# Kernel tuning notes

Hardware: AMD Instinct MI355X
Metric: run time of the kernel (lower is better)

The kernel has to match this reference:

```python
import jax, jax.numpy as jnp
import numpy as np

B = 4096
SEQ = 128            # window_size * rnn_in_pkts
WINDOW = 32
IN_PKTS = 4
LEN_V, LEN_E = 1500, 64
IPD_V, IPD_E = 256, 64
EV = 64              # embedding_vector_bits
RNN_IN = IN_PKTS * EV   # 256
H = 256              # rnn_hidden_bits
LABELS = 100


def setup_inputs() -> dict:
    key = jax.random.key(0)
    ks = jax.random.split(key, 12)
    s = 0.05
    return {
        "len_x": jax.random.randint(ks[0], (B, SEQ), 0, LEN_V),
        "ipd_x": jax.random.randint(ks[1], (B, SEQ), 0, IPD_V),
        "len_emb": jax.random.normal(ks[2], (LEN_V, LEN_E), jnp.float32) * s,
        "ipd_emb": jax.random.normal(ks[3], (IPD_V, IPD_E), jnp.float32) * s,
        "fc_w": jax.random.normal(ks[4], (EV, LEN_E + IPD_E), jnp.float32) * s,
        "fc_b": jax.random.normal(ks[5], (EV,), jnp.float32) * s,
        "w_ih": jax.random.normal(ks[6], (3 * H, RNN_IN), jnp.float32) * s,
        "w_hh": jax.random.normal(ks[7], (3 * H, H), jnp.float32) * s,
        "b_ih": jax.random.normal(ks[8], (3 * H,), jnp.float32) * s,
        "b_hh": jax.random.normal(ks[9], (3 * H,), jnp.float32) * s,
        "out_w": jax.random.normal(ks[10], (LABELS, H), jnp.float32) * s,
        "out_b": jax.random.normal(ks[11], (LABELS,), jnp.float32) * s,
    }


def _gru_scan(rnn_in, w_ih, w_hh, b_ih, b_hh):
    # rnn_in: [B, T, RNN_IN]. Precompute input-side gates for all steps at once.
    gi_all = jnp.einsum("bti,gi->btg", rnn_in, w_ih) + b_ih  # [B,T,3H]
    h0 = jnp.zeros((rnn_in.shape[0], H), rnn_in.dtype)

    def step(h, gi):
        gh = h @ w_hh.T + b_hh                 # [B,3H]
        i_r, i_z, i_n = jnp.split(gi, 3, axis=-1)
        h_r, h_z, h_n = jnp.split(gh, 3, axis=-1)
        r = jax.nn.sigmoid(i_r + h_r)
        z = jax.nn.sigmoid(i_z + h_z)
        n = jnp.tanh(i_n + r * h_n)
        h_new = (1.0 - z) * n + z * h
        return h_new, None

    h_final, _ = jax.lax.scan(step, h0, jnp.swapaxes(gi_all, 0, 1))
    return h_final


def reference(len_x, ipd_x, len_emb, ipd_emb, fc_w, fc_b, w_ih, w_hh, b_ih, b_hh, out_w, out_b):
    len_e = len_emb[len_x]                      # [B,SEQ,LEN_E]
    ipd_e = ipd_emb[ipd_x]                      # [B,SEQ,IPD_E]
    cat = jnp.concatenate([len_e, ipd_e], axis=-1)
    evs = cat @ fc_w.T + fc_b                   # [B,SEQ,EV]
    rnn_in = evs.reshape(B, WINDOW, RNN_IN)     # [B,32,256]
    h = _gru_scan(rnn_in, w_ih, w_hh, b_ih, b_hh)
    logits = h @ out_w.T + out_b                # [B,LABELS]
    return logits
```

## Files before the change

kernel.cpp:

```cpp
#include <hip/hip_runtime.h>
#include <hip/hip_bf16.h>

typedef __bf16 bf16_t;
typedef __bf16 bf16x8 __attribute__((ext_vector_type(8)));
typedef float f32x4 __attribute__((ext_vector_type(4)));
typedef unsigned short u16x4 __attribute__((ext_vector_type(4)));

#define MFMA16(a, b, c) __builtin_amdgcn_mfma_f32_16x16x32_bf16((a), (b), (c), 0, 0, 0)

#define BATCH 4096
#define SEQN 128
#define HN 256
#define NLABELS 100
#define TSTEPS 32
#define LEN_VN 1500
#define IPD_VN 256

#define OFF_LENT   0u
#define OFF_IPDT   384000u
#define OFF_WIH    449536u
#define OFF_WHH    842752u
#define OFF_GI     1235968u

__device__ __forceinline__ float sigf(float x) {
    return __builtin_amdgcn_rcpf(1.f + __expf(-x));
}
__device__ __forceinline__ float tanh_fast(float x) {
    return 2.f * __builtin_amdgcn_rcpf(1.f + __expf(-2.f * x)) - 1.f;
}
__device__ __forceinline__ float b2f(unsigned short v) {
    union { unsigned u; float f; } c; c.u = ((unsigned)v) << 16; return c.f;
}
__device__ __forceinline__ f32x4 b2f4(u16x4 v) {
    f32x4 o;
    #pragma unroll
    for (int r = 0; r < 4; ++r) o[r] = b2f(v[r]);
    return o;
}
__device__ __forceinline__ unsigned short f2b(float f) {
    union { bf16_t h; unsigned short s; } c; c.h = (bf16_t)f; return c.s;
}

__device__ __forceinline__ void barrier_lds() {
    asm volatile("s_waitcnt lgkmcnt(0)\n\ts_barrier" ::: "memory");
}
__device__ __forceinline__ void wait_vm0() {
    asm volatile("s_waitcnt vmcnt(0)" ::: "memory");
}

#define PREP_TBL_BLOCKS 110
__global__ void prep_kernel(const float* __restrict__ len_emb,
                            const float* __restrict__ ipd_emb,
                            const float* __restrict__ fc_w,
                            const float* __restrict__ fc_b,
                            const float* __restrict__ w_ih,
                            const float* __restrict__ w_hh,
                            float* __restrict__ lenT, float* __restrict__ ipdT,
                            bf16_t* __restrict__ wfrag_ih,
                            bf16_t* __restrict__ wfrag_hh) {
    const int bid = blockIdx.x, tid = threadIdx.x;
    if (bid < PREP_TBL_BLOCKS) {
        __shared__ float w_lds[64 * 132];
        __shared__ float emb_lds[16 * 64];
        const int row0 = bid * 16;

        #pragma unroll
        for (int k = 0; k < 8; ++k) {
            const int l = k * 1024 + tid * 4;
            const int e = l >> 7, j = l & 127;
            *(f32x4*)(w_lds + e * 132 + j) = *(const f32x4*)(fc_w + l);
        }
        {
            const int r = tid >> 4;
            const int c = (tid & 15) * 4;
            const int grow = row0 + r;
            f32x4 v = {};
            if (grow < LEN_VN)               v = *(const f32x4*)(len_emb + grow * 64 + c);
            else if (grow < LEN_VN + IPD_VN) v = *(const f32x4*)(ipd_emb + (grow - LEN_VN) * 64 + c);
            *(f32x4*)(emb_lds + r * 64 + c) = v;
        }
        __syncthreads();

        const int e = tid & 63;
        const int r0 = tid >> 6;
        const float* wrow_lo = w_lds + e * 132;
        #pragma unroll
        for (int rr = 0; rr < 4; ++rr) {
            const int r = r0 + rr * 4;
            const int grow = row0 + r;
            if (grow >= LEN_VN + IPD_VN) break;
            const bool is_len = grow < LEN_VN;
            const float* wrow = is_len ? wrow_lo : (wrow_lo + 64);
            f32x4 acc = {};
            #pragma unroll
            for (int c = 0; c < 16; ++c) {
                f32x4 wv = *(const f32x4*)(wrow + c * 4);
                f32x4 ev = *(const f32x4*)(emb_lds + r * 64 + c * 4);
                acc += wv * ev;
            }
            float s = acc[0] + acc[1] + acc[2] + acc[3] + (is_len ? fc_b[e] : 0.f);
            if (is_len) lenT[grow * 64 + e] = s;
            else        ipdT[(grow - LEN_VN) * 64 + e] = s;
        }
    } else {
        const int flat = (bid - PREP_TBL_BLOCKS) * 256 + tid;
        const int which = flat / 24576;
        const int rem = flat % 24576;
        const int c = rem >> 9;
        const int kt = (rem >> 6) & 7;
        const int lane = rem & 63;
        const int g = c * 16 + (lane & 15);
        const int k0 = kt * 32 + (lane >> 4) * 8;
        const float* src = (which == 0 ? w_ih : w_hh) + g * 256 + k0;
        bf16_t* dst = (which == 0 ? wfrag_ih : wfrag_hh) + ((c * 8 + kt) * 64 + lane) * 8;
        f32x4 s0 = *(const f32x4*)(src);
        f32x4 s1 = *(const f32x4*)(src + 4);
        bf16x8 o;
        #pragma unroll
        for (int j = 0; j < 4; ++j) { o[j] = (bf16_t)s0[j]; o[4 + j] = (bf16_t)s1[j]; }
        *(bf16x8*)dst = o;
    }
}

__global__ void __launch_bounds__(1024, 4)
fused_kernel(const int* __restrict__ len_x, const int* __restrict__ ipd_x,
             const float* __restrict__ lenT, const float* __restrict__ ipdT,
             const bf16_t* __restrict__ wfrag_ih,
             const bf16_t* __restrict__ wfrag_hh,
             const float* __restrict__ b_ih, const float* __restrict__ b_hh,
             bf16_t* gi,
             const float* __restrict__ out_w,
             const float* __restrict__ out_b,
             float* __restrict__ out) {
    __shared__ char smem[147456];
    bf16_t* wlds = (bf16_t*)smem;
    bf16_t* dbuf = (bf16_t*)(smem + 131072);
    float* h_fin = (float*)smem;

    const int tid = threadIdx.x;
    const int lane = tid & 63;
    const int w = tid >> 6;
    const int bt = blockIdx.x;
    const int quad = lane >> 4;
    const int b = lane & 15;

    bf16_t* gib = gi + (size_t)bt * 48 * 32 * 256 + lane * 4;
    const bf16_t* wb = &wlds[w * 8 * 512 + lane * 8];

    {
        bf16x8 wri[2][8];
        #pragma unroll
        for (int cc = 0; cc < 2; ++cc) {
            const int ct = cc * 16 + w;
            #pragma unroll
            for (int kt = 0; kt < 8; ++kt)
                wri[cc][kt] = *(const bf16x8*)(wfrag_ih + ((ct * 8 + kt) * 64 + lane) * 8);
        }
        #pragma unroll
        for (int kt = 0; kt < 8; ++kt)
            *(bf16x8*)&wlds[(w * 8 + kt) * 512 + lane * 8] =
                *(const bf16x8*)(wfrag_ih + (((32 + w) * 8 + kt) * 64 + lane) * 8);

        f32x4 bias0 = *(const f32x4*)(b_ih + w * 16 + quad * 4)
                    + *(const f32x4*)(b_hh + w * 16 + quad * 4);
        f32x4 bias1 = *(const f32x4*)(b_ih + 256 + w * 16 + quad * 4)
                    + *(const f32x4*)(b_hh + 256 + w * 16 + quad * 4);
        f32x4 bias2 = *(const f32x4*)(b_ih + 512 + w * 16 + quad * 4);

        const int sub = tid & 511;
        const int pr = sub >> 3;
        const int sub8 = sub & 7;
        const int grow = pr & 15;
        const int p = pr >> 4;
        const int e0 = sub8 * 8;
        const int b_row = bt * 16 + grow;
        const int goff = (2 * p + (sub8 >> 2)) * 512 + ((sub8 & 3) * 16 + grow) * 8;

        auto do_gather = [&](int t) {
            const int seq = t * 4 + p;
            const int v1 = len_x[b_row * SEQN + seq];
            const int v2 = ipd_x[b_row * SEQN + seq];
            const float* lp = lenT + v1 * 64 + e0;
            const float* ip = ipdT + v2 * 64 + e0;
            f32x4 a0 = *(const f32x4*)lp + *(const f32x4*)ip;
            f32x4 a1 = *(const f32x4*)(lp + 4) + *(const f32x4*)(ip + 4);
            bf16x8 o;
            #pragma unroll
            for (int j = 0; j < 4; ++j) { o[j] = (bf16_t)a0[j]; o[4 + j] = (bf16_t)a1[j]; }
            *(bf16x8*)&dbuf[(t & 1) * 4096 + goff] = o;
        };

        if (tid < 512) do_gather(0);

        for (int t = 0; t < TSTEPS; ++t) {
            barrier_lds();
            if (t + 1 < TSTEPS && tid < 512) do_gather(t + 1);

            f32x4 acc0 = bias0, acc1 = bias1, acc2 = bias2;
            const bf16_t* ab = &dbuf[(t & 1) * 4096 + lane * 8];
            #pragma unroll
            for (int kt = 0; kt < 8; ++kt) {
                bf16x8 xf = *(const bf16x8*)(ab + kt * 512);
                bf16x8 w5 = *(const bf16x8*)(wb + kt * 512);
                acc0 = MFMA16(wri[0][kt], xf, acc0);
                acc1 = MFMA16(wri[1][kt], xf, acc1);
                acc2 = MFMA16(w5, xf, acc2);
            }

            u16x4 o0, o1, o2;
            #pragma unroll
            for (int r = 0; r < 4; ++r) {
                o0[r] = f2b(acc0[r]); o1[r] = f2b(acc1[r]); o2[r] = f2b(acc2[r]);
            }
            *(u16x4*)(gib + ((size_t)(w) * 32 + t) * 256) = o0;
            *(u16x4*)(gib + ((size_t)(16 + w) * 32 + t) * 256) = o1;
            *(u16x4*)(gib + ((size_t)(32 + w) * 32 + t) * 256) = o2;
        }
    }

    barrier_lds();
    wait_vm0();

    bf16_t* h_lds = dbuf;

    bf16x8 wr[2][8];
    #pragma unroll
    for (int cc = 0; cc < 2; ++cc) {
        const int ct = cc * 16 + w;
        #pragma unroll
        for (int kt = 0; kt < 8; ++kt)
            wr[cc][kt] = *(const bf16x8*)(wfrag_hh + ((ct * 8 + kt) * 64 + lane) * 8);
    }
    #pragma unroll
    for (int kt = 0; kt < 8; ++kt)
        *(bf16x8*)&wlds[(w * 8 + kt) * 512 + lane * 8] =
            *(const bf16x8*)(wfrag_hh + (((32 + w) * 8 + kt) * 64 + lane) * 8);

    const f32x4 bhn = *(const f32x4*)(b_hh + (32 + w) * 16 + quad * 4);

    for (int i = tid; i < 4096; i += 1024) h_lds[4096 + i] = (bf16_t)0.f;

    const int j0 = 16 * w + 4 * quad;
    const int woff = (j0 >> 5) * 512 + ((((j0 >> 3) & 3)) * 16 + b) * 8 + (j0 & 7);

    u16x4 gc0 = *(const u16x4*)(gib + ((size_t)(w) * 32) * 256);
    u16x4 gc1 = *(const u16x4*)(gib + ((size_t)(16 + w) * 32) * 256);
    u16x4 gc2 = *(const u16x4*)(gib + ((size_t)(32 + w) * 32) * 256);

    f32x4 hprev = {};

    for (int t = 0; t < TSTEPS; ++t) {
        barrier_lds();

        f32x4 acc0 = b2f4(gc0);
        f32x4 acc1 = b2f4(gc1);
        f32x4 acc2 = bhn;
        u16x4 g2cur = gc2;

        if (t + 1 < TSTEPS) {
            gc0 = *(const u16x4*)(gib + ((size_t)(w) * 32 + t + 1) * 256);
            gc1 = *(const u16x4*)(gib + ((size_t)(16 + w) * 32 + t + 1) * 256);
            gc2 = *(const u16x4*)(gib + ((size_t)(32 + w) * 32 + t + 1) * 256);
        }

        const bf16_t* hb = &h_lds[((t + 1) & 1) * 4096 + lane * 8];
        #pragma unroll
        for (int kt = 0; kt < 8; ++kt) {
            bf16x8 hf = *(const bf16x8*)(hb + kt * 512);
            bf16x8 w5 = *(const bf16x8*)(wb + kt * 512);
            acc0 = MFMA16(wr[0][kt], hf, acc0);
            acc1 = MFMA16(wr[1][kt], hf, acc1);
            acc2 = MFMA16(w5, hf, acc2);
        }

        f32x4 rg, zg;
        #pragma unroll
        for (int r = 0; r < 4; ++r) { rg[r] = sigf(acc0[r]); zg[r] = sigf(acc1[r]); }
        f32x4 u = b2f4(g2cur) + rg * acc2;
        f32x4 ng;
        #pragma unroll
        for (int r = 0; r < 4; ++r) ng[r] = tanh_fast(u[r]);
        f32x4 hn = ng + zg * (hprev - ng);
        hprev = hn;

        u16x4 o;
        #pragma unroll
        for (int r = 0; r < 4; ++r) o[r] = f2b(hn[r]);
        *(u16x4*)(&h_lds[(t & 1) * 4096 + woff]) = o;
    }

    __syncthreads();

    *(f32x4*)(h_fin + b * 260 + j0) = hprev;
    __syncthreads();

    for (int i = tid; i < 16 * NLABELS; i += 1024) {
        const int row = i / NLABELS;
        const int cl = i - row * NLABELS;
        const f32x4* wrow = (const f32x4*)(out_w + cl * 256);
        const f32x4* hr = (const f32x4*)(h_fin + row * 260);
        f32x4 acc = {0.f, 0.f, 0.f, 0.f};
        #pragma unroll 4
        for (int k = 0; k < 64; ++k) acc += hr[k] * wrow[k];
        out[(bt * 16 + row) * NLABELS + cl] =
            out_b[cl] + acc[0] + acc[1] + acc[2] + acc[3];
    }
}

extern "C" void kernel_launch(void* const* d_in, const int* in_sizes, int n_in,
                              void* d_out, int out_size, void* d_ws, size_t ws_size,
                              hipStream_t stream) {
    (void)in_sizes; (void)n_in; (void)out_size; (void)ws_size;
    const int*   len_x   = (const int*)d_in[0];
    const int*   ipd_x   = (const int*)d_in[1];
    const float* len_emb = (const float*)d_in[2];
    const float* ipd_emb = (const float*)d_in[3];
    const float* fc_w    = (const float*)d_in[4];
    const float* fc_b    = (const float*)d_in[5];
    const float* w_ih    = (const float*)d_in[6];
    const float* w_hh    = (const float*)d_in[7];
    const float* b_ih    = (const float*)d_in[8];
    const float* b_hh    = (const float*)d_in[9];
    const float* out_w   = (const float*)d_in[10];
    const float* out_b   = (const float*)d_in[11];

    char* ws = (char*)d_ws;
    float*  lenT = (float*)(ws + OFF_LENT);
    float*  ipdT = (float*)(ws + OFF_IPDT);
    bf16_t* wfi  = (bf16_t*)(ws + OFF_WIH);
    bf16_t* wfh  = (bf16_t*)(ws + OFF_WHH);
    bf16_t* gi   = (bf16_t*)(ws + OFF_GI);

    prep_kernel<<<302, 256, 0, stream>>>(len_emb, ipd_emb, fc_w, fc_b,
                                         w_ih, w_hh, lenT, ipdT, wfi, wfh);
    fused_kernel<<<256, 1024, 0, stream>>>(len_x, ipd_x, lenT, ipdT, wfi, wfh,
                                           b_ih, b_hh, gi, out_w, out_b,
                                           (float*)d_out);
}
```

Baseline: 234.2 us.

## Halve workgroup to 512 threads with two hidden column tiles per wave

The fused GRU kernel now runs 8 waves per block instead of 16. Each wave covers two 16-column hidden tiles, holds five weight fragments in registers and reads one from LDS, so the LDS weight footprint and per-step barrier participants are halved. Biases are staged in LDS rather than held in registers. This raises register pressure per wave (about 80 bf16x8 weight registers plus 6 accumulators) and gives the recurrence fewer waves to hide MFMA and LDS latency, in exchange for less synchronisation and LDS traffic per step.

```diff
diff --git a/kernel.cpp b/kernel.cpp
--- a/kernel.cpp
+++ b/kernel.cpp
@@ -122,7 +122,7 @@
     }
 }
 
-__global__ void __launch_bounds__(1024, 4)
+__global__ void __launch_bounds__(512, 2)
 fused_kernel(const int* __restrict__ len_x, const int* __restrict__ ipd_x,
              const float* __restrict__ lenT, const float* __restrict__ ipdT,
              const bf16_t* __restrict__ wfrag_ih,
@@ -132,9 +132,10 @@
              const float* __restrict__ out_w,
              const float* __restrict__ out_b,
              float* __restrict__ out) {
-    __shared__ char smem[147456];
+    __shared__ char smem[86016];
     bf16_t* wlds = (bf16_t*)smem;
-    bf16_t* dbuf = (bf16_t*)(smem + 131072);
+    bf16_t* dbuf = (bf16_t*)(smem + 65536);
+    float* bias_lds = (float*)(smem + 81920);
     float* h_fin = (float*)smem;
 
     const int tid = threadIdx.x;
@@ -143,33 +144,35 @@
     const int bt = blockIdx.x;
     const int quad = lane >> 4;
     const int b = lane & 15;
+    const int c2w = 2 * w;
 
     bf16_t* gib = gi + (size_t)bt * 48 * 32 * 256 + lane * 4;
-    const bf16_t* wb = &wlds[w * 8 * 512 + lane * 8];
+    const bf16_t* wb = &wlds[w * 4096 + lane * 8];
+
+    for (int i = tid; i < 768; i += 512)
+        bias_lds[i] = b_ih[i] + (i < 512 ? b_hh[i] : 0.f);
+    for (int i = tid; i < 256; i += 512)
+        bias_lds[768 + i] = b_hh[512 + i];
 
     {
-        bf16x8 wri[2][8];
-        #pragma unroll
-        for (int cc = 0; cc < 2; ++cc) {
-            const int ct = cc * 16 + w;
+        bf16x8 wri[5][8];
+        #pragma unroll
+        for (int i = 0; i < 5; ++i) {
+            const int ct = (i >> 1) * 16 + c2w + (i & 1);
             #pragma unroll
             for (int kt = 0; kt < 8; ++kt)
-                wri[cc][kt] = *(const bf16x8*)(wfrag_ih + ((ct * 8 + kt) * 64 + lane) * 8);
-        }
-        #pragma unroll
-        for (int kt = 0; kt < 8; ++kt)
-            *(bf16x8*)&wlds[(w * 8 + kt) * 512 + lane * 8] =
-                *(const bf16x8*)(wfrag_ih + (((32 + w) * 8 + kt) * 64 + lane) * 8);
-
-        f32x4 bias0 = *(const f32x4*)(b_ih + w * 16 + quad * 4)
-                    + *(const f32x4*)(b_hh + w * 16 + quad * 4);
-        f32x4 bias1 = *(const f32x4*)(b_ih + 256 + w * 16 + quad * 4)
-                    + *(const f32x4*)(b_hh + 256 + w * 16 + quad * 4);
-        f32x4 bias2 = *(const f32x4*)(b_ih + 512 + w * 16 + quad * 4);
-
-        const int sub = tid & 511;
-        const int pr = sub >> 3;
-        const int sub8 = sub & 7;
+                wri[i][kt] = *(const bf16x8*)(wfrag_ih + ((ct * 8 + kt) * 64 + lane) * 8);
+        }
+        {
+            const int ct = 33 + c2w;
+            #pragma unroll
+            for (int kt = 0; kt < 8; ++kt)
+                *(bf16x8*)&wlds[w * 4096 + kt * 512 + lane * 8] =
+                    *(const bf16x8*)(wfrag_ih + ((ct * 8 + kt) * 64 + lane) * 8);
+        }
+
+        const int pr = tid >> 3;
+        const int sub8 = tid & 7;
         const int grow = pr & 15;
         const int p = pr >> 4;
         const int e0 = sub8 * 8;
@@ -190,31 +193,38 @@
             *(bf16x8*)&dbuf[(t & 1) * 4096 + goff] = o;
         };
 
-        if (tid < 512) do_gather(0);
+        do_gather(0);
 
         for (int t = 0; t < TSTEPS; ++t) {
             barrier_lds();
-            if (t + 1 < TSTEPS && tid < 512) do_gather(t + 1);
-
-            f32x4 acc0 = bias0, acc1 = bias1, acc2 = bias2;
+            if (t + 1 < TSTEPS) do_gather(t + 1);
+
+            f32x4 acc[6];
+            #pragma unroll
+            for (int i = 0; i < 6; ++i)
+                acc[i] = *(const f32x4*)(bias_lds + (i >> 1) * 256 + (c2w + (i & 1)) * 16 + quad * 4);
+
             const bf16_t* ab = &dbuf[(t & 1) * 4096 + lane * 8];
             #pragma unroll
             for (int kt = 0; kt < 8; ++kt) {
                 bf16x8 xf = *(const bf16x8*)(ab + kt * 512);
                 bf16x8 w5 = *(const bf16x8*)(wb + kt * 512);
-                acc0 = MFMA16(wri[0][kt], xf, acc0);
-                acc1 = MFMA16(wri[1][kt], xf, acc1);
-                acc2 = MFMA16(w5, xf, acc2);
+                acc[0] = MFMA16(wri[0][kt], xf, acc[0]);
+                acc[1] = MFMA16(wri[1][kt], xf, acc[1]);
+                acc[2] = MFMA16(wri[2][kt], xf, acc[2]);
+                acc[3] = MFMA16(wri[3][kt], xf, acc[3]);
+                acc[4] = MFMA16(wri[4][kt], xf, acc[4]);
+                acc[5] = MFMA16(w5, xf, acc[5]);
             }
 
-            u16x4 o0, o1, o2;
-            #pragma unroll
-            for (int r = 0; r < 4; ++r) {
-                o0[r] = f2b(acc0[r]); o1[r] = f2b(acc1[r]); o2[r] = f2b(acc2[r]);
+            #pragma unroll
+            for (int i = 0; i < 6; ++i) {
+                const int ct = (i >> 1) * 16 + c2w + (i & 1);
+                u16x4 o;
+                #pragma unroll
+                for (int r = 0; r < 4; ++r) o[r] = f2b(acc[i][r]);
+                *(u16x4*)(gib + ((size_t)ct * 32 + t) * 256) = o;
             }
-            *(u16x4*)(gib + ((size_t)(w) * 32 + t) * 256) = o0;
-            *(u16x4*)(gib + ((size_t)(16 + w) * 32 + t) * 256) = o1;
-            *(u16x4*)(gib + ((size_t)(32 + w) * 32 + t) * 256) = o2;
         }
     }
 
@@ -223,44 +233,54 @@
 
     bf16_t* h_lds = dbuf;
 
-    bf16x8 wr[2][8];
+    bf16x8 wr[5][8];
     #pragma unroll
-    for (int cc = 0; cc < 2; ++cc) {
-        const int ct = cc * 16 + w;
+    for (int i = 0; i < 5; ++i) {
+        const int ct = (i >> 1) * 16 + c2w + (i & 1);
         #pragma unroll
         for (int kt = 0; kt < 8; ++kt)
-            wr[cc][kt] = *(const bf16x8*)(wfrag_hh + ((ct * 8 + kt) * 64 + lane) * 8);
-    }
+            wr[i][kt] = *(const bf16x8*)(wfrag_hh + ((ct * 8 + kt) * 64 + lane) * 8);
+    }
+    {
+        const int ct = 33 + c2w;
+        #pragma unroll
+        for (int kt = 0; kt < 8; ++kt)
+            *(bf16x8*)&wlds[w * 4096 + kt * 512 + lane * 8] =
+                *(const bf16x8*)(wfrag_hh + ((ct * 8 + kt) * 64 + lane) * 8);
+    }
+
+    for (int i = tid; i < 4096; i += 512) h_lds[4096 + i] = (bf16_t)0.f;
+
+    const int j00 = (c2w + 0) * 16 + 4 * quad;
+    const int j01 = (c2w + 1) * 16 + 4 * quad;
+    const int woff0 = (j00 >> 5) * 512 + (((j00 >> 3) & 3) * 16 + b) * 8 + (j00 & 7);
+    const int woff1 = (j01 >> 5) * 512 + (((j01 >> 3) & 3) * 16 + b) * 8 + (j01 & 7);
+
+    u16x4 gc[6];
     #pragma unroll
-    for (int kt = 0; kt < 8; ++kt)
-        *(bf16x8*)&wlds[(w * 8 + kt) * 512 + lane * 8] =
-            *(const bf16x8*)(wfrag_hh + (((32 + w) * 8 + kt) * 64 + lane) * 8);
-
-    const f32x4 bhn = *(const f32x4*)(b_hh + (32 + w) * 16 + quad * 4);
-
-    for (int i = tid; i < 4096; i += 1024) h_lds[4096 + i] = (bf16_t)0.f;
-
-    const int j0 = 16 * w + 4 * quad;
-    const int woff = (j0 >> 5) * 512 + ((((j0 >> 3) & 3)) * 16 + b) * 8 + (j0 & 7);
-
-    u16x4 gc0 = *(const u16x4*)(gib + ((size_t)(w) * 32) * 256);
-    u16x4 gc1 = *(const u16x4*)(gib + ((size_t)(16 + w) * 32) * 256);
-    u16x4 gc2 = *(const u16x4*)(gib + ((size_t)(32 + w) * 32) * 256);
-
-    f32x4 hprev = {};
+    for (int i = 0; i < 6; ++i) {
+        const int ct = (i >> 1) * 16 + c2w + (i & 1);
+        gc[i] = *(const u16x4*)(gib + ((size_t)ct * 32) * 256);
+    }
+
+    f32x4 hprev0 = {}, hprev1 = {};
 
     for (int t = 0; t < TSTEPS; ++t) {
         barrier_lds();
 
-        f32x4 acc0 = b2f4(gc0);
-        f32x4 acc1 = b2f4(gc1);
-        f32x4 acc2 = bhn;
-        u16x4 g2cur = gc2;
+        f32x4 acc[6];
+        acc[0] = b2f4(gc[0]); acc[1] = b2f4(gc[1]);
+        acc[2] = b2f4(gc[2]); acc[3] = b2f4(gc[3]);
+        acc[4] = *(const f32x4*)(bias_lds + 768 + (c2w + 0) * 16 + quad * 4);
+        acc[5] = *(const f32x4*)(bias_lds + 768 + (c2w + 1) * 16 + quad * 4);
+        u16x4 g4 = gc[4], g5 = gc[5];
 
         if (t + 1 < TSTEPS) {
-            gc0 = *(const u16x4*)(gib + ((size_t)(w) * 32 + t + 1) * 256);
-            gc1 = *(const u16x4*)(gib + ((size_t)(16 + w) * 32 + t + 1) * 256);
-            gc2 = *(const u16x4*)(gib + ((size_t)(32 + w) * 32 + t + 1) * 256);
+            #pragma unroll
+            for (int i = 0; i < 6; ++i) {
+                const int ct = (i >> 1) * 16 + c2w + (i & 1);
+                gc[i] = *(const u16x4*)(gib + ((size_t)ct * 32 + t + 1) * 256);
+            }
         }
 
         const bf16_t* hb = &h_lds[((t + 1) & 1) * 4096 + lane * 8];
@@ -268,33 +288,43 @@
         for (int kt = 0; kt < 8; ++kt) {
             bf16x8 hf = *(const bf16x8*)(hb + kt * 512);
             bf16x8 w5 = *(const bf16x8*)(wb + kt * 512);
-            acc0 = MFMA16(wr[0][kt], hf, acc0);
-            acc1 = MFMA16(wr[1][kt], hf, acc1);
-            acc2 = MFMA16(w5, hf, acc2);
-        }
-
-        f32x4 rg, zg;
-        #pragma unroll
-        for (int r = 0; r < 4; ++r) { rg[r] = sigf(acc0[r]); zg[r] = sigf(acc1[r]); }
-        f32x4 u = b2f4(g2cur) + rg * acc2;
-        f32x4 ng;
-        #pragma unroll
-        for (int r = 0; r < 4; ++r) ng[r] = tanh_fast(u[r]);
-        f32x4 hn = ng + zg * (hprev - ng);
-        hprev = hn;
-
-        u16x4 o;
-        #pragma unroll
-        for (int r = 0; r < 4; ++r) o[r] = f2b(hn[r]);
-        *(u16x4*)(&h_lds[(t & 1) * 4096 + woff]) = o;
+            acc[0] = MFMA16(wr[0][kt], hf, acc[0]);
+            acc[1] = MFMA16(wr[1][kt], hf, acc[1]);
+            acc[2] = MFMA16(wr[2][kt], hf, acc[2]);
+            acc[3] = MFMA16(wr[3][kt], hf, acc[3]);
+            acc[4] = MFMA16(wr[4][kt], hf, acc[4]);
+            acc[5] = MFMA16(w5, hf, acc[5]);
+        }
+
+        f32x4 rg0, zg0, rg1, zg1;
+        #pragma unroll
+        for (int r = 0; r < 4; ++r) {
+            rg0[r] = sigf(acc[0][r]); rg1[r] = sigf(acc[1][r]);
+            zg0[r] = sigf(acc[2][r]); zg1[r] = sigf(acc[3][r]);
+        }
+        f32x4 u0 = b2f4(g4) + rg0 * acc[4];
+        f32x4 u1 = b2f4(g5) + rg1 * acc[5];
+        f32x4 ng0, ng1;
+        #pragma unroll
+        for (int r = 0; r < 4; ++r) { ng0[r] = tanh_fast(u0[r]); ng1[r] = tanh_fast(u1[r]); }
+        f32x4 h0 = ng0 + zg0 * (hprev0 - ng0);
+        f32x4 h1 = ng1 + zg1 * (hprev1 - ng1);
+        hprev0 = h0; hprev1 = h1;
+
+        u16x4 o0, o1;
+        #pragma unroll
+        for (int r = 0; r < 4; ++r) { o0[r] = f2b(h0[r]); o1[r] = f2b(h1[r]); }
+        *(u16x4*)(&h_lds[(t & 1) * 4096 + woff0]) = o0;
+        *(u16x4*)(&h_lds[(t & 1) * 4096 + woff1]) = o1;
     }
 
     __syncthreads();
 
-    *(f32x4*)(h_fin + b * 260 + j0) = hprev;
+    *(f32x4*)(h_fin + b * 260 + j00) = hprev0;
+    *(f32x4*)(h_fin + b * 260 + j01) = hprev1;
     __syncthreads();
 
-    for (int i = tid; i < 16 * NLABELS; i += 1024) {
+    for (int i = tid; i < 16 * NLABELS; i += 512) {
         const int row = i / NLABELS;
         const int cl = i - row * NLABELS;
         const f32x4* wrow = (const f32x4*)(out_w + cl * 256);
@@ -333,7 +363,7 @@
 
     prep_kernel<<<302, 256, 0, stream>>>(len_emb, ipd_emb, fc_w, fc_b,
                                          w_ih, w_hh, lenT, ipdT, wfi, wfh);
-    fused_kernel<<<256, 1024, 0, stream>>>(len_x, ipd_x, lenT, ipdT, wfi, wfh,
-                                           b_ih, b_hh, gi, out_w, out_b,
-                                           (float*)d_out);
-}
+    fused_kernel<<<256, 512, 0, stream>>>(len_x, ipd_x, lenT, ipdT, wfi, wfh,
+                                          b_ih, b_hh, gi, out_w, out_b,
+                                          (float*)d_out);
+}
```

After: 233.1 us. No clear change (-0.5%).

## Preload sequence indices to LDS and deepen gather and gi prefetch pipelines

Applied to the files above, without the earlier changes.

At kernel start, the len/ipd indices for the block's 16 rows are packed into LDS, so the per-step index reads become LDS reads instead of dependent global loads. The embedding gather now uses all 1024 threads with 4 elements each. Its global loads are issued before the MFMA loop and written to the double buffer afterwards, so their latency overlaps compute. In the recurrent phase, gi prefetch goes two steps ahead with a register ring buffer, and the vm wait is moved later. This adds LDS, which may reduce occupancy, and adds register pressure.

```diff
diff --git a/kernel.cpp b/kernel.cpp
--- a/kernel.cpp
+++ b/kernel.cpp
@@ -132,9 +132,10 @@
              const float* __restrict__ out_w,
              const float* __restrict__ out_b,
              float* __restrict__ out) {
-    __shared__ char smem[147456];
+    __shared__ char smem[155648];
     bf16_t* wlds = (bf16_t*)smem;
     bf16_t* dbuf = (bf16_t*)(smem + 131072);
+    unsigned* idxp = (unsigned*)(smem + 147456);
     float* h_fin = (float*)smem;
 
     const int tid = threadIdx.x;
@@ -147,6 +148,19 @@
     bf16_t* gib = gi + (size_t)bt * 48 * 32 * 256 + lane * 4;
     const bf16_t* wb = &wlds[w * 8 * 512 + lane * 8];
 
+    #pragma unroll
+    for (int k = 0; k < 2; ++k) {
+        const int flat = k * 1024 + tid;
+        const int row = flat >> 7, s = flat & 127;
+        const int g = (bt * 16 + row) * SEQN + s;
+        idxp[s * 16 + row] = (unsigned)len_x[g] | ((unsigned)ipd_x[g] << 16);
+    }
+
+    const int e4 = tid & 15;
+    const int grow = (tid >> 4) & 15;
+    const int p = tid >> 8;
+    const int gdst = (2 * p + (e4 >> 3)) * 512 + (((e4 >> 1) & 3) * 16 + grow) * 8 + (e4 & 1) * 4;
+
     {
         bf16x8 wri[2][8];
         #pragma unroll
@@ -167,34 +181,29 @@
                     + *(const f32x4*)(b_hh + 256 + w * 16 + quad * 4);
         f32x4 bias2 = *(const f32x4*)(b_ih + 512 + w * 16 + quad * 4);
 
-        const int sub = tid & 511;
-        const int pr = sub >> 3;
-        const int sub8 = sub & 7;
-        const int grow = pr & 15;
-        const int p = pr >> 4;
-        const int e0 = sub8 * 8;
-        const int b_row = bt * 16 + grow;
-        const int goff = (2 * p + (sub8 >> 2)) * 512 + ((sub8 & 3) * 16 + grow) * 8;
-
-        auto do_gather = [&](int t) {
-            const int seq = t * 4 + p;
-            const int v1 = len_x[b_row * SEQN + seq];
-            const int v2 = ipd_x[b_row * SEQN + seq];
-            const float* lp = lenT + v1 * 64 + e0;
-            const float* ip = ipdT + v2 * 64 + e0;
-            f32x4 a0 = *(const f32x4*)lp + *(const f32x4*)ip;
-            f32x4 a1 = *(const f32x4*)(lp + 4) + *(const f32x4*)(ip + 4);
-            bf16x8 o;
-            #pragma unroll
-            for (int j = 0; j < 4; ++j) { o[j] = (bf16_t)a0[j]; o[4 + j] = (bf16_t)a1[j]; }
-            *(bf16x8*)&dbuf[(t & 1) * 4096 + goff] = o;
-        };
-
-        if (tid < 512) do_gather(0);
+        barrier_lds();
+
+        {
+            const unsigned pk0 = idxp[p * 16 + grow];
+            const int v1 = pk0 & 0xffff, v2 = pk0 >> 16;
+            f32x4 a = *(const f32x4*)(lenT + v1 * 64 + e4 * 4)
+                    + *(const f32x4*)(ipdT + v2 * 64 + e4 * 4);
+            u16x4 o;
+            #pragma unroll
+            for (int r = 0; r < 4; ++r) o[r] = f2b(a[r]);
+            *(u16x4*)&dbuf[gdst] = o;
+        }
+        unsigned pk_cur = idxp[(4 + p) * 16 + grow];
 
         for (int t = 0; t < TSTEPS; ++t) {
             barrier_lds();
-            if (t + 1 < TSTEPS && tid < 512) do_gather(t + 1);
+
+            const int v1 = pk_cur & 0xffff, v2 = pk_cur >> 16;
+            const f32x4 ga = *(const f32x4*)(lenT + v1 * 64 + e4 * 4);
+            const f32x4 gtb = *(const f32x4*)(ipdT + v2 * 64 + e4 * 4);
+            const int tn = (t + 2 < TSTEPS) ? t + 2 : TSTEPS - 1;
+            pk_cur = idxp[(tn * 4 + p) * 16 + grow];
+            __builtin_amdgcn_sched_barrier(0);
 
             f32x4 acc0 = bias0, acc1 = bias1, acc2 = bias2;
             const bf16_t* ab = &dbuf[(t & 1) * 4096 + lane * 8];
@@ -207,6 +216,14 @@
                 acc2 = MFMA16(w5, xf, acc2);
             }
 
+            {
+                f32x4 a = ga + gtb;
+                u16x4 o;
+                #pragma unroll
+                for (int r = 0; r < 4; ++r) o[r] = f2b(a[r]);
+                *(u16x4*)&dbuf[((t + 1) & 1) * 4096 + gdst] = o;
+            }
+
             u16x4 o0, o1, o2;
             #pragma unroll
             for (int r = 0; r < 4; ++r) {
@@ -219,7 +236,6 @@
     }
 
     barrier_lds();
-    wait_vm0();
 
     bf16_t* h_lds = dbuf;
 
@@ -240,28 +256,35 @@
 
     for (int i = tid; i < 4096; i += 1024) h_lds[4096 + i] = (bf16_t)0.f;
 
+    wait_vm0();
+
+    u16x4 gc[2][3];
+    #pragma unroll
+    for (int s = 0; s < 2; ++s) {
+        gc[s][0] = *(const u16x4*)(gib + ((size_t)(w) * 32 + s) * 256);
+        gc[s][1] = *(const u16x4*)(gib + ((size_t)(16 + w) * 32 + s) * 256);
+        gc[s][2] = *(const u16x4*)(gib + ((size_t)(32 + w) * 32 + s) * 256);
+    }
+
     const int j0 = 16 * w + 4 * quad;
-    const int woff = (j0 >> 5) * 512 + ((((j0 >> 3) & 3)) * 16 + b) * 8 + (j0 & 7);
-
-    u16x4 gc0 = *(const u16x4*)(gib + ((size_t)(w) * 32) * 256);
-    u16x4 gc1 = *(const u16x4*)(gib + ((size_t)(16 + w) * 32) * 256);
-    u16x4 gc2 = *(const u16x4*)(gib + ((size_t)(32 + w) * 32) * 256);
+    const int woff = (j0 >> 5) * 512 + (((j0 >> 3) & 3) * 16 + b) * 8 + (j0 & 7);
 
     f32x4 hprev = {};
 
+    #pragma unroll 2
     for (int t = 0; t < TSTEPS; ++t) {
         barrier_lds();
-
-        f32x4 acc0 = b2f4(gc0);
-        f32x4 acc1 = b2f4(gc1);
+        const int sl = t & 1;
+
+        f32x4 acc0 = b2f4(gc[sl][0]);
+        f32x4 acc1 = b2f4(gc[sl][1]);
         f32x4 acc2 = bhn;
-        u16x4 g2cur = gc2;
-
-        if (t + 1 < TSTEPS) {
-            gc0 = *(const u16x4*)(gib + ((size_t)(w) * 32 + t + 1) * 256);
-            gc1 = *(const u16x4*)(gib + ((size_t)(16 + w) * 32 + t + 1) * 256);
-            gc2 = *(const u16x4*)(gib + ((size_t)(32 + w) * 32 + t + 1) * 256);
-        }
+        u16x4 g2cur = gc[sl][2];
+
+        const int tn = (t + 2 < TSTEPS) ? t + 2 : TSTEPS - 1;
+        gc[sl][0] = *(const u16x4*)(gib + ((size_t)(w) * 32 + tn) * 256);
+        gc[sl][1] = *(const u16x4*)(gib + ((size_t)(16 + w) * 32 + tn) * 256);
+        gc[sl][2] = *(const u16x4*)(gib + ((size_t)(32 + w) * 32 + tn) * 256);
 
         const bf16_t* hb = &h_lds[((t + 1) & 1) * 4096 + lane * 8];
         #pragma unroll
```

New measurement: 246.6 us. 5.3% more time.
